# Kernel tuning notes

Measured on AMD Instinct MI355X. Metric: run time of the kernel, lower is better.

The kernel has to match this reference:

```python
import jax, jax.numpy as jnp
import numpy as np

N, E, D, H, O, L = 50000, 400000, 128, 128, 64, 2


def setup_inputs() -> dict:
    key = jax.random.key(0)
    ks = jax.random.split(key, 24)
    s = 0.05
    rn = lambda k, shape: jax.random.normal(k, shape, jnp.float32) * s
    # random edges with no self-loops (dst = src + nonzero offset mod N)
    src = jax.random.randint(ks[0], (E,), 0, N, dtype=jnp.int32)
    off = jax.random.randint(ks[1], (E,), 1, N, dtype=jnp.int32)
    dst = (src + off) % N
    edge_index = jnp.stack([src, dst])  # [2, E] int32
    return {
        "x": rn(ks[2], (N, D)),
        "edge_index": edge_index,
        "attn_W": rn(ks[3], (L, 2 * D, 2)),
        "attn_b": rn(ks[4], (L, 2)),
        "mlp_W1": rn(ks[5], (L, D, H)),
        "mlp_b1": rn(ks[6], (L, H)),
        "mlp_W2": rn(ks[7], (L, H, H)),
        "mlp_b2": rn(ks[8], (L, H)),
        "bn_gamma": jnp.ones((L, H), jnp.float32),   # torch BatchNorm1d default affine init
        "bn_beta": jnp.zeros((L, H), jnp.float32),
        "gru_Wih": rn(ks[9], (D, 3 * H)),
        "gru_Whh": rn(ks[10], (H, 3 * H)),
        "gru_bih": rn(ks[11], (3 * H,)),
        "gru_bhh": rn(ks[12], (3 * H,)),
        "last_W1": rn(ks[13], (H, H)),
        "last_b1": rn(ks[14], (H,)),
        "last_W2": rn(ks[15], (H, O)),
        "last_b2": rn(ks[16], (O,)),
    }


def reference(x, edge_index, attn_W, attn_b, mlp_W1, mlp_b1, mlp_W2, mlp_b2,
              bn_gamma, bn_beta, gru_Wih, gru_Whh, gru_bih, gru_bhh,
              last_W1, last_b1, last_W2, last_b2):
    n = x.shape[0]
    # symmetrize edge list: message (nbr -> node) for both directions
    node = jnp.concatenate([edge_index[0], edge_index[1]])  # destination
    nbr = jnp.concatenate([edge_index[1], edge_index[0]])   # source / neighbor
    deg = jax.ops.segment_sum(jnp.ones((node.shape[0], 1), x.dtype), node, num_segments=n)
    has_nbr = deg > 0

    h_state = jnp.zeros((n, gru_Whh.shape[0]), x.dtype)
    for l in range(attn_W.shape[0]):
        feats = x[nbr]  # [2E, d] gather
        s_agg = jax.ops.segment_sum(feats, node, num_segments=n)
        m_agg = jax.ops.segment_max(feats, node, num_segments=n)
        m_agg = jnp.where(has_nbr, m_agg, jnp.zeros_like(m_agg))  # isolated nodes stay 0
        # attention over {sum, max} aggregations
        scores = jnp.concatenate([s_agg, m_agg], axis=1) @ attn_W[l] + attn_b[l]  # [n, 2]
        w = jax.nn.softmax(scores, axis=1)
        comb = x + w[:, :1] * s_agg + w[:, 1:] * m_agg
        # MLP (in -> hidden, ReLU, hidden -> out)
        z = jax.nn.relu(comb @ mlp_W1[l] + mlp_b1[l]) @ mlp_W2[l] + mlp_b2[l]
        # BatchNorm1d in eval mode with running stats (mean 0, var 1): affine only
        z = z * bn_gamma[l] + bn_beta[l]
        # GRUCell
        gi = z @ gru_Wih + gru_bih
        gh = h_state @ gru_Whh + gru_bhh
        ir, iz, inn = jnp.split(gi, 3, axis=1)
        hr, hz, hn = jnp.split(gh, 3, axis=1)
        r = jax.nn.sigmoid(ir + hr)
        u = jax.nn.sigmoid(iz + hz)
        ncand = jnp.tanh(inn + r * hn)
        h_state = (1.0 - u) * ncand + u * h_state
        x = h_state
    # final node-level MLP
    out = jax.nn.relu(x @ last_W1 + last_b1) @ last_W2 + last_b2
    return out
```

## Files before the change

kernel.cpp:

```cpp
#include <hip/hip_runtime.h>
#include <math.h>

typedef unsigned short u16;
typedef __attribute__((ext_vector_type(8))) short bf16x8;
typedef __attribute__((ext_vector_type(4))) float f32x4;

__device__ __forceinline__ u16 f2b(float f) {
    union { float f; unsigned u; } v; v.f = f;
    unsigned r = (v.u + 0x7FFF + ((v.u >> 16) & 1)) >> 16;
    return (u16)r;
}
__device__ __forceinline__ float b2f(u16 h) {
    union { unsigned u; float f; } v; v.u = (unsigned)h << 16;
    return v.f;
}
__device__ __forceinline__ float fsig(float x) { return 1.f / (1.f + __expf(-x)); }
__device__ __forceinline__ float ftanh(float x) {
    float e = __expf(2.f * x);
    return 1.f - 2.f / (e + 1.f);
}

__device__ __forceinline__ void gll16(const void* g, void* l) {
    __builtin_amdgcn_global_load_lds(
        (const __attribute__((address_space(1))) void*)g,
        (__attribute__((address_space(3))) void*)l, 16, 0, 0);
}

__global__ void k_deg(const int* __restrict__ ei, int* __restrict__ cnt, int E) {
    int e = blockIdx.x * 256 + threadIdx.x;
    if (e < E) {
        atomicAdd(&cnt[ei[e]], 1);
        atomicAdd(&cnt[ei[E + e]], 1);
    }
}

__global__ __launch_bounds__(1024) void k_scan_sum(const int* __restrict__ cnt,
                                                   int* __restrict__ part, int N) {
    __shared__ int sd[16];
    int t = threadIdx.x;
    int i = blockIdx.x * 1024 + t;
    int v = (i < N) ? cnt[i] : 0;
#pragma unroll
    for (int o = 32; o; o >>= 1) v += __shfl_xor(v, o);
    if ((t & 63) == 0) sd[t >> 6] = v;
    __syncthreads();
    if (t < 16) {
        int s = sd[t];
#pragma unroll
        for (int o = 8; o; o >>= 1) s += __shfl_xor(s, o);
        if (t == 0) part[blockIdx.x] = s;
    }
}

__global__ void k_scan_part(int* __restrict__ part, int nb) {
    int t = threadIdx.x;
    int v = (t < nb) ? part[t] : 0;
#pragma unroll
    for (int o = 1; o < 64; o <<= 1) {
        int u = __shfl_up(v, o);
        if ((t & 63) >= o) v += u;
    }
    if (t < nb) part[t] = v;
}

__global__ __launch_bounds__(1024) void k_scan_write(const int* __restrict__ cnt,
                                                     const int* __restrict__ part,
                                                     int* __restrict__ offs, int N) {
    __shared__ int sd[16];
    int t = threadIdx.x, lane = t & 63, wid = t >> 6;
    int i = blockIdx.x * 1024 + t;
    int v = (i < N) ? cnt[i] : 0;
    int inc = v;
#pragma unroll
    for (int o = 1; o < 64; o <<= 1) {
        int u = __shfl_up(inc, o);
        if (lane >= o) inc += u;
    }
    if (lane == 63) sd[wid] = inc;
    __syncthreads();
    if (wid == 0) {
        int wv = (lane < 16) ? sd[lane] : 0;
#pragma unroll
        for (int o = 1; o < 16; o <<= 1) {
            int u = __shfl_up(wv, o);
            if (lane >= o) wv += u;
        }
        if (lane < 16) sd[lane] = wv;
    }
    __syncthreads();
    int base = (blockIdx.x > 0 ? part[blockIdx.x - 1] : 0) + (wid > 0 ? sd[wid - 1] : 0);
    if (i < N) offs[i + 1] = base + inc;
    if (i == 0 && blockIdx.x == 0) offs[0] = 0;
}

__global__ void k_fill(const int* __restrict__ ei, int* __restrict__ cur,
                       u16* __restrict__ adj, int E) {
    int e = blockIdx.x * 256 + threadIdx.x;
    if (e < E) {
        int s = ei[e], d = ei[E + e];
        int p = atomicAdd(&cur[s], 1); adj[p] = (u16)d;
        int q = atomicAdd(&cur[d], 1); adj[q] = (u16)s;
    }
}

__device__ __forceinline__ void conv_chunk(const float* __restrict__ src,
                                           u16* __restrict__ dst, int c, int NC) {
    int sl = c / NC, n = c - sl * NC;
    u16 tmp[8];
#pragma unroll
    for (int i = 0; i < 8; ++i) tmp[i] = f2b(src[(size_t)(sl * 8 + i) * NC + n]);
    *(uint4*)(dst + (size_t)c * 8) = *(const uint4*)tmp;
}

__global__ void k_prep_w(const float* __restrict__ W1, const float* __restrict__ W2,
                         const float* __restrict__ Wih, const float* __restrict__ Whh,
                         const float* __restrict__ lW1, const float* __restrict__ lW2,
                         u16* __restrict__ tW1, u16* __restrict__ tW2,
                         u16* __restrict__ tGRU,
                         u16* __restrict__ tlW1, u16* __restrict__ tlW2, int L) {
    int c = blockIdx.x * 256 + threadIdx.x;
    if (c < L * 2048) { int l = c >> 11; conv_chunk(W1 + (size_t)l * 16384, tW1 + (size_t)l * 16384, c & 2047, 128); return; }
    c -= L * 2048;
    if (c < L * 2048) { int l = c >> 11; conv_chunk(W2 + (size_t)l * 16384, tW2 + (size_t)l * 16384, c & 2047, 128); return; }
    c -= L * 2048;
    if (c < 12288) {
        int s = c >> 9, r = c & 511;
        int q = r >> 7, mat = (r >> 6) & 1, cc = r & 63;
        int h = s / 12, s2 = s % 12, kc = s2 / 3, g = s2 % 3;
        int ocol = g * 128 + h * 64 + cc;
        const float* src = mat ? Whh : Wih;
        int kb = (kc * 4 + q) * 8;
        u16 tmp[8];
#pragma unroll
        for (int e = 0; e < 8; ++e) tmp[e] = f2b(src[(size_t)(kb + e) * 384 + ocol]);
        *(uint4*)(tGRU + (size_t)c * 8) = *(const uint4*)tmp;
        return;
    }
    c -= 12288;
    if (c < 2048) { conv_chunk(lW1, tlW1, c, 128); return; }
    c -= 2048;
    if (c < 1024) { conv_chunk(lW2, tlW2, c, 64); return; }
}

__global__ void k_f2b(const float* __restrict__ src, u16* __restrict__ dst, int n8) {
    int i = blockIdx.x * 256 + threadIdx.x;
    if (i < n8) {
        float4 a = *(const float4*)(src + (size_t)i * 8);
        float4 b = *(const float4*)(src + (size_t)i * 8 + 4);
        u16 t[8] = {f2b(a.x), f2b(a.y), f2b(a.z), f2b(a.w),
                    f2b(b.x), f2b(b.y), f2b(b.z), f2b(b.w)};
        *(uint4*)(dst + (size_t)i * 8) = *(const uint4*)t;
    }
}

__global__ __launch_bounds__(256) void k_agg(const u16* __restrict__ xb,
                                             const u16* __restrict__ adj,
                                             const int* __restrict__ offs,
                                             const float* __restrict__ aW,
                                             const float* __restrict__ ab,
                                             u16* __restrict__ comb, int N) {
    int n = blockIdx.x * 4 + (threadIdx.x >> 6);
    if (n >= N) return;
    int l = threadIdx.x & 63;
    int half = l >> 5, e0 = (l & 31) * 4;
    int beg = offs[n], end = offs[n + 1];
    float s0 = 0.f, s1 = 0.f, s2 = 0.f, s3 = 0.f;
    float m0 = -3.402823e38f, m1 = m0, m2 = m0, m3 = m0;
    int j = beg + half;
    for (; j + 6 < end; j += 8) {
        int a0 = adj[j], a1 = adj[j + 2], a2 = adj[j + 4], a3 = adj[j + 6];
        ushort4 v0 = *(const ushort4*)(xb + (size_t)a0 * 128 + e0);
        ushort4 v1 = *(const ushort4*)(xb + (size_t)a1 * 128 + e0);
        ushort4 v2 = *(const ushort4*)(xb + (size_t)a2 * 128 + e0);
        ushort4 v3 = *(const ushort4*)(xb + (size_t)a3 * 128 + e0);
        float f0, f1, f2, f3;
        f0 = b2f(v0.x); f1 = b2f(v0.y); f2 = b2f(v0.z); f3 = b2f(v0.w);
        s0 += f0; s1 += f1; s2 += f2; s3 += f3;
        m0 = fmaxf(m0, f0); m1 = fmaxf(m1, f1); m2 = fmaxf(m2, f2); m3 = fmaxf(m3, f3);
        f0 = b2f(v1.x); f1 = b2f(v1.y); f2 = b2f(v1.z); f3 = b2f(v1.w);
        s0 += f0; s1 += f1; s2 += f2; s3 += f3;
        m0 = fmaxf(m0, f0); m1 = fmaxf(m1, f1); m2 = fmaxf(m2, f2); m3 = fmaxf(m3, f3);
        f0 = b2f(v2.x); f1 = b2f(v2.y); f2 = b2f(v2.z); f3 = b2f(v2.w);
        s0 += f0; s1 += f1; s2 += f2; s3 += f3;
        m0 = fmaxf(m0, f0); m1 = fmaxf(m1, f1); m2 = fmaxf(m2, f2); m3 = fmaxf(m3, f3);
        f0 = b2f(v3.x); f1 = b2f(v3.y); f2 = b2f(v3.z); f3 = b2f(v3.w);
        s0 += f0; s1 += f1; s2 += f2; s3 += f3;
        m0 = fmaxf(m0, f0); m1 = fmaxf(m1, f1); m2 = fmaxf(m2, f2); m3 = fmaxf(m3, f3);
    }
    for (; j < end; j += 2) {
        int nb = adj[j];
        ushort4 v = *(const ushort4*)(xb + (size_t)nb * 128 + e0);
        float f0 = b2f(v.x), f1 = b2f(v.y), f2 = b2f(v.z), f3 = b2f(v.w);
        s0 += f0; s1 += f1; s2 += f2; s3 += f3;
        m0 = fmaxf(m0, f0); m1 = fmaxf(m1, f1); m2 = fmaxf(m2, f2); m3 = fmaxf(m3, f3);
    }
    s0 += __shfl_xor(s0, 32); m0 = fmaxf(m0, __shfl_xor(m0, 32));
    s1 += __shfl_xor(s1, 32); m1 = fmaxf(m1, __shfl_xor(m1, 32));
    s2 += __shfl_xor(s2, 32); m2 = fmaxf(m2, __shfl_xor(m2, 32));
    s3 += __shfl_xor(s3, 32); m3 = fmaxf(m3, __shfl_xor(m3, 32));
    if (beg == end) { m0 = m1 = m2 = m3 = 0.f; }
    float p0 = 0.f, p1 = 0.f;
    {
        float2 w0v = *(const float2*)(aW + (size_t)e0 * 2);
        float2 w1v = *(const float2*)(aW + (size_t)(e0 + 1) * 2);
        float2 w2v = *(const float2*)(aW + (size_t)(e0 + 2) * 2);
        float2 w3v = *(const float2*)(aW + (size_t)(e0 + 3) * 2);
        float2 u0v = *(const float2*)(aW + (size_t)(128 + e0) * 2);
        float2 u1v = *(const float2*)(aW + (size_t)(128 + e0 + 1) * 2);
        float2 u2v = *(const float2*)(aW + (size_t)(128 + e0 + 2) * 2);
        float2 u3v = *(const float2*)(aW + (size_t)(128 + e0 + 3) * 2);
        p0 = s0 * w0v.x + s1 * w1v.x + s2 * w2v.x + s3 * w3v.x
           + m0 * u0v.x + m1 * u1v.x + m2 * u2v.x + m3 * u3v.x;
        p1 = s0 * w0v.y + s1 * w1v.y + s2 * w2v.y + s3 * w3v.y
           + m0 * u0v.y + m1 * u1v.y + m2 * u2v.y + m3 * u3v.y;
    }
#pragma unroll
    for (int o = 16; o; o >>= 1) { p0 += __shfl_xor(p0, o); p1 += __shfl_xor(p1, o); }
    p0 += ab[0]; p1 += ab[1];
    float pm = fmaxf(p0, p1);
    float ea = __expf(p0 - pm), eb = __expf(p1 - pm);
    float w0 = ea / (ea + eb), w1 = 1.f - w0;
    if (half == 0) {
        ushort4 xv = *(const ushort4*)(xb + (size_t)n * 128 + e0);
        ushort4 o;
        o.x = f2b(b2f(xv.x) + w0 * s0 + w1 * m0);
        o.y = f2b(b2f(xv.y) + w0 * s1 + w1 * m1);
        o.z = f2b(b2f(xv.z) + w0 * s2 + w1 * m2);
        o.w = f2b(b2f(xv.w) + w0 * s3 + w1 * m3);
        *(ushort4*)(comb + (size_t)n * 128 + e0) = o;
    }
}

template <bool H0, bool WF32>
__global__ __launch_bounds__(256, 4) void k_layer(
    const u16* __restrict__ Cb, const u16* __restrict__ Hb,
    const float* __restrict__ Hf,
    const u16* __restrict__ W1t, const float* __restrict__ b1,
    const u16* __restrict__ W2t, const float* __restrict__ b2,
    const float* __restrict__ gam, const float* __restrict__ bet,
    const u16* __restrict__ tG,
    const float* __restrict__ bih, const float* __restrict__ bhh,
    float* __restrict__ HnF, u16* __restrict__ HnB, int M) {
    __shared__ __align__(16) u16 x_s[64 * 16 * 8];
    __shared__ __align__(16) u16 b_s[2][4096];
    const int t = threadIdx.x;
    const int m0 = blockIdx.x * 64;
    const int wid = t >> 6, lane = t & 63, lo = lane & 15, hi = lane >> 4;
    const int arow = 16 * wid + lo;

    auto issue = [&](int s) {
        const u16* g = (s < 4) ? (W1t + (size_t)s * 4096)
                     : (s < 8) ? (W2t + (size_t)(s - 4) * 4096)
                               : (tG + (size_t)(s - 8) * 4096);
        char* l = (char*)b_s[s & 1] + wid * 2048;
        const char* gp = (const char*)g + wid * 2048 + lane * 16;
        gll16(gp, l);
        gll16(gp + 1024, l + 1024);
    };

#pragma unroll
    for (int i = 0; i < 4; ++i) {
        int off = (i * 4 + wid) * 1024;
        int row = (off >> 8) + (lane >> 4);
        int s = lane & 15;
        int gr = m0 + row; gr = gr < M ? gr : M - 1;
        gll16(Cb + (size_t)gr * 128 + ((s ^ (row & 7)) * 8), (char*)x_s + off);
    }
    bf16x8 hreg[4];
    if (!H0) {
        int gr = m0 + arow; gr = gr < M ? gr : M - 1;
#pragma unroll
        for (int kc = 0; kc < 4; ++kc)
            hreg[kc] = *(const bf16x8*)(Hb + (size_t)gr * 128 + (kc * 4 + hi) * 8);
    }
    issue(0);
    __syncthreads();

    f32x4 acc[8];
#pragma unroll
    for (int j = 0; j < 8; ++j) acc[j] = (f32x4)0.f;
#pragma unroll
    for (int ks = 0; ks < 4; ++ks) {
        issue(ks + 1);
        bf16x8 af = *(const bf16x8*)&x_s[(arow * 16 + ((ks * 4 + hi) ^ (arow & 7))) * 8];
        const u16* buf = b_s[ks & 1];
#pragma unroll
        for (int j = 0; j < 8; ++j) {
            bf16x8 bf = *(const bf16x8*)&buf[((size_t)hi * 128 + 16 * j + lo) * 8];
            acc[j] = __builtin_amdgcn_mfma_f32_16x16x32_bf16(af, bf, acc[j], 0, 0, 0);
        }
        __syncthreads();
    }

#pragma unroll
    for (int ks = 0; ks < 4; ++ks) {
        issue(5 + ks);
        if (ks == 0) {
#pragma unroll
            for (int j = 0; j < 8; ++j) {
                int c = 16 * j + lo;
                float bv = b1[c];
#pragma unroll
                for (int q = 0; q < 4; ++q) {
                    int row = 16 * wid + hi * 4 + q;
                    float v = fmaxf(acc[j][q] + bv, 0.f);
                    int sl = c >> 3;
                    x_s[(row * 16 + (sl ^ (row & 7))) * 8 + (c & 7)] = f2b(v);
                }
                acc[j] = (f32x4)0.f;
            }
        }
        bf16x8 af = *(const bf16x8*)&x_s[(arow * 16 + ((ks * 4 + hi) ^ (arow & 7))) * 8];
        const u16* buf = b_s[ks & 1];
#pragma unroll
        for (int j = 0; j < 8; ++j) {
            bf16x8 bf = *(const bf16x8*)&buf[((size_t)hi * 128 + 16 * j + lo) * 8];
            acc[j] = __builtin_amdgcn_mfma_f32_16x16x32_bf16(af, bf, acc[j], 0, 0, 0);
        }
        __syncthreads();
    }

    f32x4 racc[4], uacc[4], nza[4], nha[4];

    auto epi = [&](int h) {
#pragma unroll
        for (int ct = 0; ct < 4; ++ct) {
            int c = h * 64 + ct * 16 + lo;
            float b_r = bih[c] + bhh[c];
            float b_u = bih[c + 128] + bhh[c + 128];
            float b_in = bih[c + 256], b_hn = bhh[c + 256];
#pragma unroll
            for (int q = 0; q < 4; ++q) {
                int r = m0 + 16 * wid + hi * 4 + q;
                if (r < M) {
                    float rr = fsig(racc[ct][q] + b_r);
                    float uu = fsig(uacc[ct][q] + b_u);
                    float hterm = H0 ? b_hn : (nha[ct][q] + b_hn);
                    float nn = ftanh(nza[ct][q] + b_in + rr * hterm);
                    float hv = H0 ? 0.f : Hf[(size_t)r * 128 + c];
                    float o = (1.f - uu) * nn + uu * hv;
                    if (WF32) HnF[(size_t)r * 128 + c] = o;
                    HnB[(size_t)r * 128 + c] = f2b(o);
                }
            }
        }
    };

#pragma unroll
    for (int h = 0; h < 2; ++h) {
#pragma unroll
        for (int kc = 0; kc < 4; ++kc) {
            bf16x8 zf;
#pragma unroll
            for (int g = 0; g < 3; ++g) {
                const int p = 8 + h * 12 + kc * 3 + g;
                if (p < 31) issue(p + 1);
                if (p == 8) {
#pragma unroll
                    for (int j = 0; j < 8; ++j) {
                        int c = 16 * j + lo;
                        float bv = b2[c], gv = gam[c], tv = bet[c];
#pragma unroll
                        for (int q = 0; q < 4; ++q) {
                            int row = 16 * wid + hi * 4 + q;
                            float v = (acc[j][q] + bv) * gv + tv;
                            int sl = c >> 3;
                            x_s[(row * 16 + (sl ^ (row & 7))) * 8 + (c & 7)] = f2b(v);
                        }
                    }
                }
                if (p == 20) epi(0);
                if (p == 8 || p == 20) {
#pragma unroll
                    for (int j = 0; j < 4; ++j) {
                        racc[j] = (f32x4)0.f; uacc[j] = (f32x4)0.f;
                        nza[j] = (f32x4)0.f; nha[j] = (f32x4)0.f;
                    }
                }
                if (g == 0)
                    zf = *(const bf16x8*)&x_s[(arow * 16 + ((kc * 4 + hi) ^ (arow & 7))) * 8];
                const u16* buf = b_s[p & 1];
#pragma unroll
                for (int jj = 0; jj < 4; ++jj) {
                    bf16x8 wi = *(const bf16x8*)&buf[((size_t)hi * 128 + jj * 16 + lo) * 8];
                    if (g == 0)      racc[jj] = __builtin_amdgcn_mfma_f32_16x16x32_bf16(zf, wi, racc[jj], 0, 0, 0);
                    else if (g == 1) uacc[jj] = __builtin_amdgcn_mfma_f32_16x16x32_bf16(zf, wi, uacc[jj], 0, 0, 0);
                    else             nza[jj]  = __builtin_amdgcn_mfma_f32_16x16x32_bf16(zf, wi, nza[jj], 0, 0, 0);
                    if (!H0) {
                        bf16x8 wh = *(const bf16x8*)&buf[((size_t)hi * 128 + 64 + jj * 16 + lo) * 8];
                        if (g == 0)      racc[jj] = __builtin_amdgcn_mfma_f32_16x16x32_bf16(hreg[kc], wh, racc[jj], 0, 0, 0);
                        else if (g == 1) uacc[jj] = __builtin_amdgcn_mfma_f32_16x16x32_bf16(hreg[kc], wh, uacc[jj], 0, 0, 0);
                        else             nha[jj]  = __builtin_amdgcn_mfma_f32_16x16x32_bf16(hreg[kc], wh, nha[jj], 0, 0, 0);
                    }
                }
                if (p < 31) __syncthreads();
            }
        }
    }
    epi(1);
}

__global__ __launch_bounds__(256, 2) void k_final(const u16* __restrict__ Hb,
                                                  const u16* __restrict__ W1t,
                                                  const float* __restrict__ b1,
                                                  const u16* __restrict__ W2t,
                                                  const float* __restrict__ b2,
                                                  float* __restrict__ out, int M) {
    __shared__ __align__(16) u16 x_s[64 * 16 * 8];
    __shared__ __align__(16) u16 w_s[16 * 128 * 8];
    const int t = threadIdx.x;
    const int m0 = blockIdx.x * 64;
    const int w = t >> 6, l = t & 63, lo = l & 15, hi = l >> 4;
    const int arow = 16 * w + lo;
#pragma unroll
    for (int i = 0; i < 4; ++i) {
        int idx = t + i * 256;
        int row = idx >> 4, sl = idx & 15;
        int gr = m0 + row; gr = gr < M ? gr : M - 1;
        *(uint4*)&x_s[(row * 16 + (sl ^ (row & 7))) * 8] =
            *(const uint4*)(Hb + (size_t)gr * 128 + sl * 8);
    }
#pragma unroll
    for (int i = 0; i < 8; ++i) {
        int idx = t + i * 256;
        *(uint4*)&w_s[idx * 8] = *(const uint4*)(W1t + (size_t)idx * 8);
    }
    __syncthreads();
    f32x4 acc[8];
#pragma unroll
    for (int j = 0; j < 8; ++j) acc[j] = (f32x4)0.f;
#pragma unroll
    for (int ks = 0; ks < 4; ++ks) {
        bf16x8 af = *(const bf16x8*)&x_s[(arow * 16 + ((ks * 4 + hi) ^ (arow & 7))) * 8];
#pragma unroll
        for (int j = 0; j < 8; ++j) {
            bf16x8 bf = *(const bf16x8*)&w_s[((ks * 4 + hi) * 128 + 16 * j + lo) * 8];
            acc[j] = __builtin_amdgcn_mfma_f32_16x16x32_bf16(af, bf, acc[j], 0, 0, 0);
        }
    }
    __syncthreads();
#pragma unroll
    for (int j = 0; j < 8; ++j) {
        int c = 16 * j + lo;
        float bv = b1[c];
#pragma unroll
        for (int q = 0; q < 4; ++q) {
            int row = 16 * w + hi * 4 + q;
            float v = fmaxf(acc[j][q] + bv, 0.f);
            int sl = c >> 3;
            x_s[(row * 16 + (sl ^ (row & 7))) * 8 + (c & 7)] = f2b(v);
        }
    }
#pragma unroll
    for (int i = 0; i < 4; ++i) {
        int idx = t + i * 256;
        *(uint4*)&w_s[idx * 8] = *(const uint4*)(W2t + (size_t)idx * 8);
    }
    __syncthreads();
    f32x4 a2[4];
#pragma unroll
    for (int j = 0; j < 4; ++j) a2[j] = (f32x4)0.f;
#pragma unroll
    for (int ks = 0; ks < 4; ++ks) {
        bf16x8 af = *(const bf16x8*)&x_s[(arow * 16 + ((ks * 4 + hi) ^ (arow & 7))) * 8];
#pragma unroll
        for (int j = 0; j < 4; ++j) {
            bf16x8 bf = *(const bf16x8*)&w_s[((ks * 4 + hi) * 64 + 16 * j + lo) * 8];
            a2[j] = __builtin_amdgcn_mfma_f32_16x16x32_bf16(af, bf, a2[j], 0, 0, 0);
        }
    }
#pragma unroll
    for (int j = 0; j < 4; ++j) {
        int c = 16 * j + lo;
        float bv = b2[c];
#pragma unroll
        for (int q = 0; q < 4; ++q) {
            int r = m0 + 16 * w + hi * 4 + q;
            if (r < M) out[(size_t)r * 64 + c] = a2[j][q] + bv;
        }
    }
}

extern "C" void kernel_launch(void* const* d_in, const int* in_sizes, int n_in,
                              void* d_out, int out_size, void* d_ws, size_t ws_size,
                              hipStream_t stream) {
    const float* x   = (const float*)d_in[0];
    const int*   ei  = (const int*)d_in[1];
    const float* aW  = (const float*)d_in[2];
    const float* ab  = (const float*)d_in[3];
    const float* W1  = (const float*)d_in[4];
    const float* b1  = (const float*)d_in[5];
    const float* W2  = (const float*)d_in[6];
    const float* b2  = (const float*)d_in[7];
    const float* gam = (const float*)d_in[8];
    const float* bet = (const float*)d_in[9];
    const float* Wih = (const float*)d_in[10];
    const float* Whh = (const float*)d_in[11];
    const float* bih = (const float*)d_in[12];
    const float* bhh = (const float*)d_in[13];
    const float* lW1 = (const float*)d_in[14];
    const float* lb1 = (const float*)d_in[15];
    const float* lW2 = (const float*)d_in[16];
    const float* lb2 = (const float*)d_in[17];

    const int N = in_sizes[0] / 128;
    const int E = in_sizes[1] / 2;
    const int L = in_sizes[3] / 2;
    float* out = (float*)d_out;

    char* ws = (char*)d_ws;
    size_t off = 0;
    auto alloc = [&](size_t bytes) -> void* {
        void* p = ws + off;
        off = (off + bytes + 255) & ~(size_t)255;
        return p;
    };
    int* offs = (int*)alloc((size_t)(N + 1) * 4);
    int* cur  = (int*)alloc((size_t)N * 4);
    int* part = (int*)alloc(64 * 4);
    u16* adj  = (u16*)alloc((size_t)2 * E * 2);
    u16* tW1  = (u16*)alloc((size_t)L * 16384 * 2);
    u16* tW2  = (u16*)alloc((size_t)L * 16384 * 2);
    u16* tGRU = (u16*)alloc((size_t)98304 * 2);
    u16* tlW1 = (u16*)alloc((size_t)16384 * 2);
    u16* tlW2 = (u16*)alloc((size_t)8192 * 2);
    u16* xb   = (u16*)alloc((size_t)N * 128 * 2);
    u16* comb = (u16*)alloc((size_t)N * 128 * 2);
    float* hF = (float*)alloc((size_t)N * 128 * 4);
    u16* hAb  = (u16*)alloc((size_t)N * 128 * 2);
    u16* hBb  = (u16*)alloc((size_t)N * 128 * 2);
    (void)ws_size; (void)n_in; (void)out_size;

    hipMemsetAsync(cur, 0, (size_t)N * 4, stream);

    int wchunks = L * 4096 + 12288 + 3072;
    k_prep_w<<<(wchunks + 255) / 256, 256, 0, stream>>>(W1, W2, Wih, Whh, lW1, lW2,
                                                        tW1, tW2, tGRU, tlW1, tlW2, L);
    k_f2b<<<(N * 16 + 255) / 256, 256, 0, stream>>>(x, xb, N * 16);

    k_deg<<<(E + 255) / 256, 256, 0, stream>>>(ei, cur, E);
    int nb = (N + 1023) / 1024;
    k_scan_sum<<<nb, 1024, 0, stream>>>(cur, part, N);
    k_scan_part<<<1, 64, 0, stream>>>(part, nb);
    k_scan_write<<<nb, 1024, 0, stream>>>(cur, part, offs, N);
    hipMemcpyAsync(cur, offs, (size_t)N * 4, hipMemcpyDeviceToDevice, stream);
    k_fill<<<(E + 255) / 256, 256, 0, stream>>>(ei, cur, adj, E);

    const int mb = (N + 63) / 64;
    k_agg<<<(N + 3) / 4, 256, 0, stream>>>(xb, adj, offs, aW, ab, comb, N);
    k_layer<true, true><<<mb, 256, 0, stream>>>(
        comb, nullptr, nullptr, tW1, b1, tW2, b2, gam, bet,
        tGRU, bih, bhh, hF, hAb, N);
    k_agg<<<(N + 3) / 4, 256, 0, stream>>>(hAb, adj, offs, aW + 512, ab + 2, comb, N);
    k_layer<false, false><<<mb, 256, 0, stream>>>(
        comb, hAb, hF, tW1 + 16384, b1 + 128, tW2 + 16384, b2 + 128,
        gam + 128, bet + 128, tGRU, bih, bhh, nullptr, hBb, N);

    k_final<<<(N + 63) / 64, 256, 0, stream>>>(hBb, tlW1, lb1, tlW2, lb2, out, N);
}
```

Baseline: 267.7 us.

## Triple-buffer weight staging in fused layer kernel and deepen gather unroll

The fused MLP+GRU layer kernel now stages weight slices in three LDS buffers with prefetch distance two. Each stage uses explicit vmcnt waits plus raw barriers in place of a full __syncthreads per stage, and LDS fragments are loaded into registers before the MFMAs are issued. Bias, gamma and beta are preloaded into registers, and the BatchNorm affine is folded into a single FMA. The aggregation kernel also issues eight neighbor gathers per iteration instead of four to raise memory-level parallelism. The cost is more LDS and register use, which may lower occupancy, and hand-written waitcnt logic that is harder to keep correct.

```diff
diff --git a/kernel.cpp b/kernel.cpp
--- a/kernel.cpp
+++ b/kernel.cpp
@@ -167,25 +167,20 @@
     float s0 = 0.f, s1 = 0.f, s2 = 0.f, s3 = 0.f;
     float m0 = -3.402823e38f, m1 = m0, m2 = m0, m3 = m0;
     int j = beg + half;
-    for (; j + 6 < end; j += 8) {
-        int a0 = adj[j], a1 = adj[j + 2], a2 = adj[j + 4], a3 = adj[j + 6];
-        ushort4 v0 = *(const ushort4*)(xb + (size_t)a0 * 128 + e0);
-        ushort4 v1 = *(const ushort4*)(xb + (size_t)a1 * 128 + e0);
-        ushort4 v2 = *(const ushort4*)(xb + (size_t)a2 * 128 + e0);
-        ushort4 v3 = *(const ushort4*)(xb + (size_t)a3 * 128 + e0);
-        float f0, f1, f2, f3;
-        f0 = b2f(v0.x); f1 = b2f(v0.y); f2 = b2f(v0.z); f3 = b2f(v0.w);
-        s0 += f0; s1 += f1; s2 += f2; s3 += f3;
-        m0 = fmaxf(m0, f0); m1 = fmaxf(m1, f1); m2 = fmaxf(m2, f2); m3 = fmaxf(m3, f3);
-        f0 = b2f(v1.x); f1 = b2f(v1.y); f2 = b2f(v1.z); f3 = b2f(v1.w);
-        s0 += f0; s1 += f1; s2 += f2; s3 += f3;
-        m0 = fmaxf(m0, f0); m1 = fmaxf(m1, f1); m2 = fmaxf(m2, f2); m3 = fmaxf(m3, f3);
-        f0 = b2f(v2.x); f1 = b2f(v2.y); f2 = b2f(v2.z); f3 = b2f(v2.w);
-        s0 += f0; s1 += f1; s2 += f2; s3 += f3;
-        m0 = fmaxf(m0, f0); m1 = fmaxf(m1, f1); m2 = fmaxf(m2, f2); m3 = fmaxf(m3, f3);
-        f0 = b2f(v3.x); f1 = b2f(v3.y); f2 = b2f(v3.z); f3 = b2f(v3.w);
-        s0 += f0; s1 += f1; s2 += f2; s3 += f3;
-        m0 = fmaxf(m0, f0); m1 = fmaxf(m1, f1); m2 = fmaxf(m2, f2); m3 = fmaxf(m3, f3);
+    for (; j + 14 < end; j += 16) {
+        ushort4 v[8];
+#pragma unroll
+        for (int u = 0; u < 8; ++u) {
+            int a = adj[j + 2 * u];
+            v[u] = *(const ushort4*)(xb + (size_t)a * 128 + e0);
+        }
+#pragma unroll
+        for (int u = 0; u < 8; ++u) {
+            float f0 = b2f(v[u].x), f1 = b2f(v[u].y), f2 = b2f(v[u].z), f3 = b2f(v[u].w);
+            s0 += f0; s1 += f1; s2 += f2; s3 += f3;
+            m0 = fmaxf(m0, f0); m1 = fmaxf(m1, f1);
+            m2 = fmaxf(m2, f2); m3 = fmaxf(m3, f3);
+        }
     }
     for (; j < end; j += 2) {
         int nb = adj[j];
@@ -242,7 +237,7 @@
     const float* __restrict__ bih, const float* __restrict__ bhh,
     float* __restrict__ HnF, u16* __restrict__ HnB, int M) {
     __shared__ __align__(16) u16 x_s[64 * 16 * 8];
-    __shared__ __align__(16) u16 b_s[2][4096];
+    __shared__ __align__(16) u16 b_s[3][4096];
     const int t = threadIdx.x;
     const int m0 = blockIdx.x * 64;
     const int wid = t >> 6, lane = t & 63, lo = lane & 15, hi = lane >> 4;
@@ -252,20 +247,31 @@
         const u16* g = (s < 4) ? (W1t + (size_t)s * 4096)
                      : (s < 8) ? (W2t + (size_t)(s - 4) * 4096)
                                : (tG + (size_t)(s - 8) * 4096);
-        char* l = (char*)b_s[s & 1] + wid * 2048;
+        char* l = (char*)b_s[s % 3] + wid * 2048;
         const char* gp = (const char*)g + wid * 2048 + lane * 16;
         gll16(gp, l);
         gll16(gp + 1024, l + 1024);
     };
 
+    float b1r[8], g2r[8], t2r[8];
+#pragma unroll
+    for (int j = 0; j < 8; ++j) {
+        int c = 16 * j + lo;
+        b1r[j] = b1[c];
+        float gv = gam[c];
+        g2r[j] = gv;
+        t2r[j] = b2[c] * gv + bet[c];
+    }
 #pragma unroll
     for (int i = 0; i < 4; ++i) {
         int off = (i * 4 + wid) * 1024;
         int row = (off >> 8) + (lane >> 4);
-        int s = lane & 15;
+        int sl = lane & 15;
         int gr = m0 + row; gr = gr < M ? gr : M - 1;
-        gll16(Cb + (size_t)gr * 128 + ((s ^ (row & 7)) * 8), (char*)x_s + off);
-    }
+        gll16(Cb + (size_t)gr * 128 + ((sl ^ (row & 7)) * 8), (char*)x_s + off);
+    }
+    issue(0);
+    issue(1);
     bf16x8 hreg[4];
     if (!H0) {
         int gr = m0 + arow; gr = gr < M ? gr : M - 1;
@@ -273,51 +279,70 @@
         for (int kc = 0; kc < 4; ++kc)
             hreg[kc] = *(const bf16x8*)(Hb + (size_t)gr * 128 + (kc * 4 + hi) * 8);
     }
-    issue(0);
-    __syncthreads();
 
     f32x4 acc[8];
 #pragma unroll
     for (int j = 0; j < 8; ++j) acc[j] = (f32x4)0.f;
+
 #pragma unroll
     for (int ks = 0; ks < 4; ++ks) {
-        issue(ks + 1);
+        const int p = ks;
+        asm volatile("s_waitcnt vmcnt(2)" ::: "memory");
+        __builtin_amdgcn_s_barrier();
         bf16x8 af = *(const bf16x8*)&x_s[(arow * 16 + ((ks * 4 + hi) ^ (arow & 7))) * 8];
-        const u16* buf = b_s[ks & 1];
-#pragma unroll
-        for (int j = 0; j < 8; ++j) {
-            bf16x8 bf = *(const bf16x8*)&buf[((size_t)hi * 128 + 16 * j + lo) * 8];
-            acc[j] = __builtin_amdgcn_mfma_f32_16x16x32_bf16(af, bf, acc[j], 0, 0, 0);
-        }
-        __syncthreads();
+        const u16* buf = b_s[p % 3];
+        bf16x8 bfr[8];
+#pragma unroll
+        for (int j = 0; j < 8; ++j)
+            bfr[j] = *(const bf16x8*)&buf[((size_t)hi * 128 + 16 * j + lo) * 8];
+        issue(p + 2);
+        asm volatile("s_waitcnt lgkmcnt(0)" ::: "memory");
+        __builtin_amdgcn_sched_barrier(0);
+#pragma unroll
+        for (int j = 0; j < 8; ++j)
+            acc[j] = __builtin_amdgcn_mfma_f32_16x16x32_bf16(af, bfr[j], acc[j], 0, 0, 0);
+    }
+#pragma unroll
+    for (int j = 0; j < 8; ++j) {
+        int c = 16 * j + lo;
+#pragma unroll
+        for (int q = 0; q < 4; ++q) {
+            int row = 16 * wid + hi * 4 + q;
+            float v = fmaxf(acc[j][q] + b1r[j], 0.f);
+            int sl = c >> 3;
+            x_s[(row * 16 + (sl ^ (row & 7))) * 8 + (c & 7)] = f2b(v);
+        }
+        acc[j] = (f32x4)0.f;
     }
 
 #pragma unroll
     for (int ks = 0; ks < 4; ++ks) {
-        issue(5 + ks);
-        if (ks == 0) {
-#pragma unroll
-            for (int j = 0; j < 8; ++j) {
-                int c = 16 * j + lo;
-                float bv = b1[c];
-#pragma unroll
-                for (int q = 0; q < 4; ++q) {
-                    int row = 16 * wid + hi * 4 + q;
-                    float v = fmaxf(acc[j][q] + bv, 0.f);
-                    int sl = c >> 3;
-                    x_s[(row * 16 + (sl ^ (row & 7))) * 8 + (c & 7)] = f2b(v);
-                }
-                acc[j] = (f32x4)0.f;
-            }
-        }
+        const int p = 4 + ks;
+        asm volatile("s_waitcnt vmcnt(2)" ::: "memory");
+        __builtin_amdgcn_s_barrier();
         bf16x8 af = *(const bf16x8*)&x_s[(arow * 16 + ((ks * 4 + hi) ^ (arow & 7))) * 8];
-        const u16* buf = b_s[ks & 1];
-#pragma unroll
-        for (int j = 0; j < 8; ++j) {
-            bf16x8 bf = *(const bf16x8*)&buf[((size_t)hi * 128 + 16 * j + lo) * 8];
-            acc[j] = __builtin_amdgcn_mfma_f32_16x16x32_bf16(af, bf, acc[j], 0, 0, 0);
-        }
-        __syncthreads();
+        const u16* buf = b_s[p % 3];
+        bf16x8 bfr[8];
+#pragma unroll
+        for (int j = 0; j < 8; ++j)
+            bfr[j] = *(const bf16x8*)&buf[((size_t)hi * 128 + 16 * j + lo) * 8];
+        issue(p + 2);
+        asm volatile("s_waitcnt lgkmcnt(0)" ::: "memory");
+        __builtin_amdgcn_sched_barrier(0);
+#pragma unroll
+        for (int j = 0; j < 8; ++j)
+            acc[j] = __builtin_amdgcn_mfma_f32_16x16x32_bf16(af, bfr[j], acc[j], 0, 0, 0);
+    }
+#pragma unroll
+    for (int j = 0; j < 8; ++j) {
+        int c = 16 * j + lo;
+#pragma unroll
+        for (int q = 0; q < 4; ++q) {
+            int row = 16 * wid + hi * 4 + q;
+            float v = acc[j][q] * g2r[j] + t2r[j];
+            int sl = c >> 3;
+            x_s[(row * 16 + (sl ^ (row & 7))) * 8 + (c & 7)] = f2b(v);
+        }
     }
 
     f32x4 racc[4], uacc[4], nza[4], nha[4];
@@ -349,55 +374,47 @@
 #pragma unroll
     for (int h = 0; h < 2; ++h) {
 #pragma unroll
+        for (int j = 0; j < 4; ++j) {
+            racc[j] = (f32x4)0.f; uacc[j] = (f32x4)0.f;
+            nza[j] = (f32x4)0.f; nha[j] = (f32x4)0.f;
+        }
+#pragma unroll
         for (int kc = 0; kc < 4; ++kc) {
-            bf16x8 zf;
+            bf16x8 zf = *(const bf16x8*)&x_s[(arow * 16 + ((kc * 4 + hi) ^ (arow & 7))) * 8];
 #pragma unroll
             for (int g = 0; g < 3; ++g) {
                 const int p = 8 + h * 12 + kc * 3 + g;
-                if (p < 31) issue(p + 1);
-                if (p == 8) {
-#pragma unroll
-                    for (int j = 0; j < 8; ++j) {
-                        int c = 16 * j + lo;
-                        float bv = b2[c], gv = gam[c], tv = bet[c];
-#pragma unroll
-                        for (int q = 0; q < 4; ++q) {
-                            int row = 16 * wid + hi * 4 + q;
-                            float v = (acc[j][q] + bv) * gv + tv;
-                            int sl = c >> 3;
-                            x_s[(row * 16 + (sl ^ (row & 7))) * 8 + (c & 7)] = f2b(v);
-                        }
+                if (p == 31) asm volatile("s_waitcnt vmcnt(0)" ::: "memory");
+                else         asm volatile("s_waitcnt vmcnt(2)" ::: "memory");
+                __builtin_amdgcn_s_barrier();
+                const u16* buf = b_s[p % 3];
+                bf16x8 wi[4], wh[4];
+#pragma unroll
+                for (int jj = 0; jj < 4; ++jj) {
+                    wi[jj] = *(const bf16x8*)&buf[((size_t)hi * 128 + jj * 16 + lo) * 8];
+                    if (!H0)
+                        wh[jj] = *(const bf16x8*)&buf[((size_t)hi * 128 + 64 + jj * 16 + lo) * 8];
+                }
+                if (p + 2 <= 31) issue(p + 2);
+                asm volatile("s_waitcnt lgkmcnt(0)" ::: "memory");
+                __builtin_amdgcn_sched_barrier(0);
+#pragma unroll
+                for (int jj = 0; jj < 4; ++jj) {
+                    if (g == 0) {
+                        racc[jj] = __builtin_amdgcn_mfma_f32_16x16x32_bf16(zf, wi[jj], racc[jj], 0, 0, 0);
+                        if (!H0) racc[jj] = __builtin_amdgcn_mfma_f32_16x16x32_bf16(hreg[kc], wh[jj], racc[jj], 0, 0, 0);
+                    } else if (g == 1) {
+                        uacc[jj] = __builtin_amdgcn_mfma_f32_16x16x32_bf16(zf, wi[jj], uacc[jj], 0, 0, 0);
+                        if (!H0) uacc[jj] = __builtin_amdgcn_mfma_f32_16x16x32_bf16(hreg[kc], wh[jj], uacc[jj], 0, 0, 0);
+                    } else {
+                        nza[jj] = __builtin_amdgcn_mfma_f32_16x16x32_bf16(zf, wi[jj], nza[jj], 0, 0, 0);
+                        if (!H0) nha[jj] = __builtin_amdgcn_mfma_f32_16x16x32_bf16(hreg[kc], wh[jj], nha[jj], 0, 0, 0);
                     }
                 }
-                if (p == 20) epi(0);
-                if (p == 8 || p == 20) {
-#pragma unroll
-                    for (int j = 0; j < 4; ++j) {
-                        racc[j] = (f32x4)0.f; uacc[j] = (f32x4)0.f;
-                        nza[j] = (f32x4)0.f; nha[j] = (f32x4)0.f;
-                    }
-                }
-                if (g == 0)
-                    zf = *(const bf16x8*)&x_s[(arow * 16 + ((kc * 4 + hi) ^ (arow & 7))) * 8];
-                const u16* buf = b_s[p & 1];
-#pragma unroll
-                for (int jj = 0; jj < 4; ++jj) {
-                    bf16x8 wi = *(const bf16x8*)&buf[((size_t)hi * 128 + jj * 16 + lo) * 8];
-                    if (g == 0)      racc[jj] = __builtin_amdgcn_mfma_f32_16x16x32_bf16(zf, wi, racc[jj], 0, 0, 0);
-                    else if (g == 1) uacc[jj] = __builtin_amdgcn_mfma_f32_16x16x32_bf16(zf, wi, uacc[jj], 0, 0, 0);
-                    else             nza[jj]  = __builtin_amdgcn_mfma_f32_16x16x32_bf16(zf, wi, nza[jj], 0, 0, 0);
-                    if (!H0) {
-                        bf16x8 wh = *(const bf16x8*)&buf[((size_t)hi * 128 + 64 + jj * 16 + lo) * 8];
-                        if (g == 0)      racc[jj] = __builtin_amdgcn_mfma_f32_16x16x32_bf16(hreg[kc], wh, racc[jj], 0, 0, 0);
-                        else if (g == 1) uacc[jj] = __builtin_amdgcn_mfma_f32_16x16x32_bf16(hreg[kc], wh, uacc[jj], 0, 0, 0);
-                        else             nha[jj]  = __builtin_amdgcn_mfma_f32_16x16x32_bf16(hreg[kc], wh, nha[jj], 0, 0, 0);
-                    }
-                }
-                if (p < 31) __syncthreads();
             }
         }
-    }
-    epi(1);
+        epi(h);
+    }
 }
 
 __global__ __launch_bounds__(256, 2) void k_final(const u16* __restrict__ Hb,
```

New measurement: 290.5 us. 8.5% more time.
